# Optimization experiments

Measured on AMD Instinct MI355X. Metric: run time of the kernel, lower is better.

The kernel has to match this reference:

```python
import jax, jax.numpy as jnp
from jax import lax
import numpy as np

SEQ, BATCH, H, L = 4096, 64, 512, 2


def setup_inputs() -> dict:
    key = jax.random.key(0)
    ks = jax.random.split(key, 9)
    s = 1.0 / np.sqrt(H)  # PyTorch GRU init scale
    return {
        "x": jax.random.normal(ks[0], (SEQ, BATCH, 1), dtype=jnp.float32),
        "w_ih0": jax.random.normal(ks[1], (3 * H, 1), dtype=jnp.float32) * s,
        "w_hh0": jax.random.normal(ks[2], (3 * H, H), dtype=jnp.float32) * s,
        "b_ih0": jax.random.normal(ks[3], (3 * H,), dtype=jnp.float32) * s,
        "b_hh0": jax.random.normal(ks[4], (3 * H,), dtype=jnp.float32) * s,
        "w_ih1": jax.random.normal(ks[5], (3 * H, H), dtype=jnp.float32) * s,
        "w_hh1": jax.random.normal(ks[6], (3 * H, H), dtype=jnp.float32) * s,
        "b_ih1": jax.random.normal(ks[7], (3 * H,), dtype=jnp.float32) * s,
        "b_hh1": jax.random.normal(ks[8], (3 * H,), dtype=jnp.float32) * s,
    }


def _gru_layer(x_seq, w_ih, w_hh, b_ih, b_hh):
    """One GRU layer over time. x_seq: (T,B,I). Returns (outputs (T,B,H), h_T (B,H))."""
    h_dim = w_hh.shape[1]
    # Precompute input-side gate pre-activations for all timesteps (one big GEMM).
    gx = jnp.einsum('tbi,gi->tbg', x_seq, w_ih) + b_ih  # (T,B,3H)
    h0 = jnp.zeros((x_seq.shape[1], h_dim), dtype=x_seq.dtype)

    def step(h, gxt):
        gh = h @ w_hh.T + b_hh  # (B,3H)
        r = jax.nn.sigmoid(gxt[:, :h_dim] + gh[:, :h_dim])
        z = jax.nn.sigmoid(gxt[:, h_dim:2 * h_dim] + gh[:, h_dim:2 * h_dim])
        n = jnp.tanh(gxt[:, 2 * h_dim:] + r * gh[:, 2 * h_dim:])
        h_new = (1.0 - z) * n + z * h
        return h_new, h_new

    h_last, ys = lax.scan(step, h0, gx)
    return ys, h_last


def reference(x, w_ih0, w_hh0, b_ih0, b_hh0, w_ih1, w_hh1, b_ih1, b_hh1):
    y0, h0f = _gru_layer(x, w_ih0, w_hh0, b_ih0, b_hh0)
    _, h1f = _gru_layer(y0, w_ih1, w_hh1, b_ih1, b_hh1)
    # hidden: (num_layers, batch, hidden). Dropout is identity in eval mode.
    return jnp.stack([h0f, h1f], axis=0)
```

## Files before the change

### kernel.cpp

```cpp
#include <hip/hip_runtime.h>
#include <math.h>


#define TT 4096
#define BB 64
#define HH 512
#define NWG 256
#define PADU 32
#define HB32 (HH * BB)

typedef __attribute__((ext_vector_type(8))) short bf16x8;
typedef __attribute__((ext_vector_type(4))) float f32x4;
typedef unsigned long long ull;

#define MFMA16(a, b, c) __builtin_amdgcn_mfma_f32_16x16x32_bf16((a), (b), (c), 0, 0, 0)
#define RIDX(c) ((((c) >> 4) * 17) + ((c) & 15))

__device__ __forceinline__ float sigm(float v) { return 1.0f / (1.0f + expf(-v)); }

__device__ __forceinline__ unsigned aldu(const unsigned* p) {
    return __hip_atomic_load((unsigned*)p, __ATOMIC_RELAXED, __HIP_MEMORY_SCOPE_AGENT);
}
__device__ __forceinline__ void astu(unsigned* p, unsigned v) {
    __hip_atomic_store(p, v, __ATOMIC_RELAXED, __HIP_MEMORY_SCOPE_AGENT);
}
__device__ __forceinline__ ull ald64(const ull* p) {
    return __hip_atomic_load((ull*)p, __ATOMIC_RELAXED, __HIP_MEMORY_SCOPE_AGENT);
}
__device__ __forceinline__ unsigned short rneb(float f) {
    unsigned u = __float_as_uint(f);
    return (unsigned short)((u + 0x7fffu + ((u >> 16) & 1u)) >> 16);
}
__device__ __forceinline__ float bfhi_f(unsigned p) { return __uint_as_float(p & 0xffff0000u); }
__device__ __forceinline__ float bflo_f(unsigned p) { return __uint_as_float(p << 16); }

union frag_u { unsigned u[4]; bf16x8 v; };
__device__ __forceinline__ bf16x8 mkfrag(unsigned a, unsigned b, unsigned c, unsigned d) {
    frag_u x; x.u[0] = a; x.u[1] = b; x.u[2] = c; x.u[3] = d; return x.v;
}
__device__ __forceinline__ void wait_fence() {
    __builtin_amdgcn_sched_barrier(0);
    asm volatile("" ::: "memory");
}

__global__ __launch_bounds__(256) void zero_k(unsigned* p, int n) {
    int i = blockIdx.x * 256 + threadIdx.x;
    if (i < n) p[i] = 0u;
}

__global__ __launch_bounds__(256) void prep_aw0(const float* __restrict__ whh0,
                                                unsigned short* __restrict__ aw0) {
    int gid = blockIdx.x * 256 + threadIdx.x;
    if (gid >= 96 * 16 * 2 * 64) return;
    int lane = gid & 63, split = (gid >> 6) & 1, kt = (gid >> 7) & 15, rt = gid >> 11;
    int grow = (rt >> 5) * 512 + (rt & 31) * 16 + (lane & 15);
    int k0 = kt * 32 + (lane >> 4) * 8;
    #pragma unroll
    for (int i = 0; i < 8; ++i) {
        float val = whh0[(size_t)grow * 512 + k0 + i];
        unsigned short hb = rneb(val);
        unsigned short us = hb;
        if (split) us = rneb(val - __uint_as_float(((unsigned)hb) << 16));
        aw0[(size_t)gid * 8 + i] = us;
    }
}

__global__ __launch_bounds__(256) void prep_aw1(const float* __restrict__ wih1,
                                                const float* __restrict__ whh1,
                                                unsigned short* __restrict__ aw1) {
    int gid = blockIdx.x * 256 + threadIdx.x;
    if (gid >= 96 * 32 * 2 * 64) return;
    int lane = gid & 63, split = (gid >> 6) & 1, kt = (gid >> 7) & 31, rt = gid >> 12;
    int grow = (rt >> 5) * 512 + (rt & 31) * 16 + (lane & 15);
    #pragma unroll
    for (int i = 0; i < 8; ++i) {
        int k = kt * 32 + (lane >> 4) * 8 + i;
        float val = (k < 512) ? wih1[(size_t)grow * 512 + k]
                              : whh1[(size_t)grow * 512 + (k - 512)];
        unsigned short hb = rneb(val);
        unsigned short us = hb;
        if (split) us = rneb(val - __uint_as_float(((unsigned)hb) << 16));
        aw1[(size_t)gid * 8 + i] = us;
    }
}

#define ISSUE_KT(buf, src64, ktr)                                               \
    {                                                                           \
        _Pragma("unroll")                                                       \
        for (int i = 0; i < 4; ++i)                                             \
            buf[i] = ald64((src64) + ((ktr) * 16 + (l >> 4) * 4 + i) * 64       \
                           + bcol0);                                            \
    }

#define COMPUTE_KT(buf, kk)                                                     \
    {                                                                           \
        unsigned p0 = (unsigned)buf[0], p1 = (unsigned)(buf[0] >> 32);          \
        unsigned p2 = (unsigned)buf[1], p3 = (unsigned)(buf[1] >> 32);          \
        unsigned p4 = (unsigned)buf[2], p5 = (unsigned)(buf[2] >> 32);          \
        unsigned p6 = (unsigned)buf[3], p7 = (unsigned)(buf[3] >> 32);          \
        bf16x8 Bh = mkfrag(__builtin_amdgcn_perm(p1, p0, 0x07060302u),          \
                           __builtin_amdgcn_perm(p3, p2, 0x07060302u),          \
                           __builtin_amdgcn_perm(p5, p4, 0x07060302u),          \
                           __builtin_amdgcn_perm(p7, p6, 0x07060302u));         \
        bf16x8 Bl = mkfrag(__builtin_amdgcn_perm(p1, p0, 0x05040100u),          \
                           __builtin_amdgcn_perm(p3, p2, 0x05040100u),          \
                           __builtin_amdgcn_perm(p5, p4, 0x05040100u),          \
                           __builtin_amdgcn_perm(p7, p6, 0x05040100u));         \
        _Pragma("unroll")                                                       \
        for (int g = 0; g < 3; ++g) {                                           \
            acc[g] = MFMA16(wA[kk][g][0], Bh, acc[g]);                          \
            acc[g] = MFMA16(wA[kk][g][0], Bl, acc[g]);                          \
            acc[g] = MFMA16(wA[kk][g][1], Bh, acc[g]);                          \
        }                                                                       \
    }

__global__ __launch_bounds__(512, 1) void gru_persist(
    const float* __restrict__ x,
    const float* __restrict__ wih0,
    const float* __restrict__ bih0, const float* __restrict__ bhh0,
    const float* __restrict__ bih1, const float* __restrict__ bhh1,
    unsigned* __restrict__ ws)
{
    __shared__ float red[8][3][272];

    unsigned* r0 = ws;
    unsigned* r1 = ws + 4 * HB32;
    unsigned* flags = ws + 8 * HB32;
    const bf16x8* aw0f = (const bf16x8*)(ws + 8 * HB32 + NWG * PADU);
    const bf16x8* aw1f = aw0f + (size_t)96 * 16 * 2 * 64;

    const int tid = threadIdx.x;
    const int l   = tid & 63;
    const int w   = tid >> 6;
    const int id  = blockIdx.x;
    const int layer = id >> 7;
    const int jt  = (id >> 2) & 31;
    const int bq  = id & 3;
    const int bcol0 = bq * 16 + (l & 15);

    const int jl_e = tid >> 4;
    const int ce   = tid & 15;
    const int b_e  = bq * 16 + ce;
    const int rg_e = jl_e & 3;
    const int l_r  = ((jl_e >> 2) << 4) | ce;
    const int c_e  = RIDX(l_r * 4 + rg_e);
    const int jj   = jt * 16 + jl_e;
    const int hidx = ((jj >> 1) * 64 + b_e) * 2 + (jj & 1);

    unsigned fprod = 0, fguard = 0;

    if (layer == 0) {
        bf16x8 wA[2][3][2];
        #pragma unroll
        for (int kk = 0; kk < 2; ++kk)
            #pragma unroll
            for (int g = 0; g < 3; ++g)
                #pragma unroll
                for (int s = 0; s < 2; ++s)
                    wA[kk][g][s] = aw0f[(size_t)(((g * 32 + jt) * 16 + (2 * w + kk)) * 2 + s) * 64 + l];

        const float wir = wih0[jj], wiz = wih0[512 + jj], win = wih0[1024 + jj];
        const float br  = bih0[jj] + bhh0[jj];
        const float bz  = bih0[512 + jj] + bhh0[512 + jj];
        const float bnx = bih0[1024 + jj], bnh = bhh0[1024 + jj];

        for (int t = 0; t < TT; ++t) {
            const unsigned* hin  = r0 + ((t + 3) & 3) * HB32;
            unsigned*       hout = r0 + (t & 3) * HB32;
            const ull* hin64 = (const ull*)hin;

            unsigned po = aldu(hin + hidx);
            const float xv = x[(size_t)t * BB + b_e];

            if (l < 4) {
                const unsigned need = (unsigned)t;
                while (fprod < need) {
                    fprod = aldu(&flags[((4 * w + l) * 4 + bq) * PADU]);
                    if (fprod < need) __builtin_amdgcn_s_sleep(1);
                }
            }
            wait_fence();

            f32x4 acc[3];
            #pragma unroll
            for (int g = 0; g < 3; ++g) acc[g] = (f32x4){0.f, 0.f, 0.f, 0.f};

            ull bbA[4], bbB[4];
            ISSUE_KT(bbA, hin64, 2 * w)
            ISSUE_KT(bbB, hin64, 2 * w + 1)
            COMPUTE_KT(bbA, 0)
            COMPUTE_KT(bbB, 1)

            if (w == 4) {
                unsigned ng; int fidx;
                if (l < 32) { ng = (t >= 2) ? (unsigned)(t - 2) : 0u; fidx = l * 4 + bq; }
                else        { ng = (t >= 3) ? (unsigned)(t - 3) : 0u; fidx = 128 + (l - 32) * 4 + bq; }
                while (fguard < ng) {
                    fguard = aldu(&flags[fidx * PADU]);
                    if (fguard < ng) __builtin_amdgcn_s_sleep(1);
                }
            }
            wait_fence();

            #pragma unroll
            for (int g = 0; g < 3; ++g)
                *(f32x4*)&red[w][g][RIDX(l * 4)] = acc[g];
            __syncthreads();

            if (tid < 256) {
                float sr = 0.f, sz = 0.f, sn = 0.f;
                #pragma unroll
                for (int p = 0; p < 8; ++p) {
                    sr += red[p][0][c_e];
                    sz += red[p][1][c_e];
                    sn += red[p][2][c_e];
                }
                float r = sigm(xv * wir + br + sr);
                float z = sigm(xv * wiz + bz + sz);
                float n = tanhf(xv * win + bnx + r * (sn + bnh));
                float hn = (1.0f - z) * n + z * (bfhi_f(po) + bflo_f(po));
                unsigned hb = rneb(hn);
                unsigned lb = rneb(hn - __uint_as_float(hb << 16));
                astu(hout + hidx, (hb << 16) | lb);
            }
            __syncthreads();
            if (tid == 0) astu(&flags[id * PADU], (unsigned)(t + 1));
        }
    } else {
        bf16x8 wA[4][3][2];
        #pragma unroll
        for (int kk = 0; kk < 4; ++kk)
            #pragma unroll
            for (int g = 0; g < 3; ++g)
                #pragma unroll
                for (int s = 0; s < 2; ++s)
                    wA[kk][g][s] = aw1f[(size_t)(((g * 32 + jt) * 32 + (4 * w + kk)) * 2 + s) * 64 + l];

        const float br  = bih1[jj] + bhh1[jj];
        const float bz  = bih1[512 + jj] + bhh1[512 + jj];
        const float bnx = bih1[1024 + jj], bnh = bhh1[1024 + jj];
        const bool xside = (w < 4);

        for (int t = 1; t <= TT; ++t) {
            const unsigned* y0  = r0 + ((t + 3) & 3) * HB32;
            const unsigned* h1p = r1 + ((t + 2) & 3) * HB32;
            unsigned*       h1o = r1 + ((t + 3) & 3) * HB32;
            const ull* src64 = (const ull*)(xside ? y0 : h1p);
            const int kb = xside ? (4 * w) : (4 * (w - 4));

            unsigned po = aldu(h1p + hidx);

            if (l < 8) {
                unsigned need; int fidx;
                if (xside) { need = (unsigned)t;       fidx = (8 * w + l) * 4 + bq; }
                else       { need = (unsigned)(t - 1); fidx = 128 + (8 * (w - 4) + l) * 4 + bq; }
                while (fprod < need) {
                    fprod = aldu(&flags[fidx * PADU]);
                    if (fprod < need) __builtin_amdgcn_s_sleep(1);
                }
            }
            wait_fence();

            f32x4 acc[3];
            #pragma unroll
            for (int g = 0; g < 3; ++g) acc[g] = (f32x4){0.f, 0.f, 0.f, 0.f};

            ull bb0[4], bb1[4], bb2[4], bb3[4];
            ISSUE_KT(bb0, src64, kb + 0)
            ISSUE_KT(bb1, src64, kb + 1)
            ISSUE_KT(bb2, src64, kb + 2)
            ISSUE_KT(bb3, src64, kb + 3)
            COMPUTE_KT(bb0, 0)
            COMPUTE_KT(bb1, 1)
            COMPUTE_KT(bb2, 2)
            COMPUTE_KT(bb3, 3)

            if (w == 4 && l < 32) {
                const unsigned ng = (t >= 3) ? (unsigned)(t - 3) : 0u;
                while (fguard < ng) {
                    fguard = aldu(&flags[(128 + l * 4 + bq) * PADU]);
                    if (fguard < ng) __builtin_amdgcn_s_sleep(1);
                }
            }
            wait_fence();

            #pragma unroll
            for (int g = 0; g < 3; ++g)
                *(f32x4*)&red[w][g][RIDX(l * 4)] = acc[g];
            __syncthreads();

            if (tid < 256) {
                float sr = 0.f, sz = 0.f, sx = 0.f, sh = 0.f;
                #pragma unroll
                for (int p = 0; p < 4; ++p) {
                    sr += red[p][0][c_e];
                    sz += red[p][1][c_e];
                    sx += red[p][2][c_e];
                }
                #pragma unroll
                for (int p = 4; p < 8; ++p) {
                    sr += red[p][0][c_e];
                    sz += red[p][1][c_e];
                    sh += red[p][2][c_e];
                }
                float r = sigm(sr + br);
                float z = sigm(sz + bz);
                float n = tanhf(sx + bnx + r * (sh + bnh));
                float hn = (1.0f - z) * n + z * (bfhi_f(po) + bflo_f(po));
                unsigned hb = rneb(hn);
                unsigned lb = rneb(hn - __uint_as_float(hb << 16));
                astu(h1o + hidx, (hb << 16) | lb);
            }
            __syncthreads();
            if (tid == 0) astu(&flags[id * PADU], (unsigned)t);
        }
    }
}

__global__ __launch_bounds__(256) void copy_out_k(const unsigned* __restrict__ ws,
                                                  float* __restrict__ out) {
    int i = blockIdx.x * 256 + threadIdx.x;
    int lyr = i >> 15;
    int rem = i & 32767;
    int b = rem >> 9;
    int j = rem & 511;
    unsigned p = ws[(size_t)lyr * 4 * HB32 + 3 * HB32 + ((j >> 1) * 64 + b) * 2 + (j & 1)];
    out[i] = bfhi_f(p) + bflo_f(p);
}

extern "C" void kernel_launch(void* const* d_in, const int* in_sizes, int n_in,
                              void* d_out, int out_size, void* d_ws, size_t ws_size,
                              hipStream_t stream)
{
    const float* x    = (const float*)d_in[0];
    const float* wih0 = (const float*)d_in[1];
    const float* whh0 = (const float*)d_in[2];
    const float* bih0 = (const float*)d_in[3];
    const float* bhh0 = (const float*)d_in[4];
    const float* wih1 = (const float*)d_in[5];
    const float* whh1 = (const float*)d_in[6];
    const float* bih1 = (const float*)d_in[7];
    const float* bhh1 = (const float*)d_in[8];
    float* out = (float*)d_out;
    unsigned* ws = (unsigned*)d_ws;

    unsigned short* aw0 = (unsigned short*)(ws + 8 * HB32 + NWG * PADU);
    unsigned short* aw1 = aw0 + (size_t)96 * 16 * 2 * 64 * 8;

    const int nzero = 8 * HB32 + NWG * PADU;
    zero_k<<<(nzero + 255) / 256, 256, 0, stream>>>(ws, nzero);
    prep_aw0<<<(96 * 16 * 2 * 64) / 256, 256, 0, stream>>>(whh0, aw0);
    prep_aw1<<<(96 * 32 * 2 * 64) / 256, 256, 0, stream>>>(wih1, whh1, aw1);
    gru_persist<<<NWG, 512, 0, stream>>>(x, wih0, bih0, bhh0, bih1, bhh1, ws);
    copy_out_k<<<(2 * BB * HH) / 256, 256, 0, stream>>>(ws, out);
}
```

Baseline: 10.00 ms.

## Use per-wave completion flags and double-buffered LDS to drop trailing block barrier

Each of the four epilogue waves now publishes its own progress flag after draining its stores, instead of the whole block hitting a second __syncthreads and thread 0 writing one flag. Consumers poll four flags per producer block. The LDS reduction buffer is double-buffered by timestep parity so that removing the trailing barrier does not let the next step's partial sums overwrite data still being read. The goal is to shorten the per-step critical path in this persistent recurrent kernel, at the cost of four times more flag polling traffic and twice the LDS.

```diff
diff --git a/kernel.cpp b/kernel.cpp
--- a/kernel.cpp
+++ b/kernel.cpp
@@ -6,6 +6,7 @@
 #define BB 64
 #define HH 512
 #define NWG 256
+#define NFLAG (NWG * 4)
 #define PADU 32
 #define HB32 (HH * BB)
 
@@ -121,12 +122,12 @@
     const float* __restrict__ bih1, const float* __restrict__ bhh1,
     unsigned* __restrict__ ws)
 {
-    __shared__ float red[8][3][272];
+    __shared__ float red[2][8][3][272];
 
     unsigned* r0 = ws;
     unsigned* r1 = ws + 4 * HB32;
     unsigned* flags = ws + 8 * HB32;
-    const bf16x8* aw0f = (const bf16x8*)(ws + 8 * HB32 + NWG * PADU);
+    const bf16x8* aw0f = (const bf16x8*)(ws + 8 * HB32 + NFLAG * PADU);
     const bf16x8* aw1f = aw0f + (size_t)96 * 16 * 2 * 64;
 
     const int tid = threadIdx.x;
@@ -168,14 +169,16 @@
             const unsigned* hin  = r0 + ((t + 3) & 3) * HB32;
             unsigned*       hout = r0 + (t & 3) * HB32;
             const ull* hin64 = (const ull*)hin;
+            float (*redc)[3][272] = red[t & 1];
 
             unsigned po = aldu(hin + hidx);
             const float xv = x[(size_t)t * BB + b_e];
 
-            if (l < 4) {
+            if (l < 16) {
                 const unsigned need = (unsigned)t;
+                const int fidx = (((4 * w + (l >> 2)) * 4 + bq) * 4 + (l & 3)) * PADU;
                 while (fprod < need) {
-                    fprod = aldu(&flags[((4 * w + l) * 4 + bq) * PADU]);
+                    fprod = aldu(&flags[fidx]);
                     if (fprod < need) __builtin_amdgcn_s_sleep(1);
                 }
             }
@@ -193,8 +196,8 @@
 
             if (w == 4) {
                 unsigned ng; int fidx;
-                if (l < 32) { ng = (t >= 2) ? (unsigned)(t - 2) : 0u; fidx = l * 4 + bq; }
-                else        { ng = (t >= 3) ? (unsigned)(t - 3) : 0u; fidx = 128 + (l - 32) * 4 + bq; }
+                if (l < 32) { ng = (t >= 2) ? (unsigned)(t - 2) : 0u; fidx = (l * 4 + bq) * 4; }
+                else        { ng = (t >= 3) ? (unsigned)(t - 3) : 0u; fidx = ((128 + (l - 32) * 4 + bq)) * 4; }
                 while (fguard < ng) {
                     fguard = aldu(&flags[fidx * PADU]);
                     if (fguard < ng) __builtin_amdgcn_s_sleep(1);
@@ -204,16 +207,16 @@
 
             #pragma unroll
             for (int g = 0; g < 3; ++g)
-                *(f32x4*)&red[w][g][RIDX(l * 4)] = acc[g];
+                *(f32x4*)&redc[w][g][RIDX(l * 4)] = acc[g];
             __syncthreads();
 
             if (tid < 256) {
                 float sr = 0.f, sz = 0.f, sn = 0.f;
                 #pragma unroll
                 for (int p = 0; p < 8; ++p) {
-                    sr += red[p][0][c_e];
-                    sz += red[p][1][c_e];
-                    sn += red[p][2][c_e];
+                    sr += redc[p][0][c_e];
+                    sz += redc[p][1][c_e];
+                    sn += redc[p][2][c_e];
                 }
                 float r = sigm(xv * wir + br + sr);
                 float z = sigm(xv * wiz + bz + sz);
@@ -222,9 +225,9 @@
                 unsigned hb = rneb(hn);
                 unsigned lb = rneb(hn - __uint_as_float(hb << 16));
                 astu(hout + hidx, (hb << 16) | lb);
-            }
-            __syncthreads();
-            if (tid == 0) astu(&flags[id * PADU], (unsigned)(t + 1));
+                asm volatile("s_waitcnt vmcnt(0)" ::: "memory");
+                if (l == 0) astu(&flags[((id * 4) + w) * PADU], (unsigned)(t + 1));
+            }
         }
     } else {
         bf16x8 wA[4][3][2];
@@ -247,15 +250,17 @@
             unsigned*       h1o = r1 + ((t + 3) & 3) * HB32;
             const ull* src64 = (const ull*)(xside ? y0 : h1p);
             const int kb = xside ? (4 * w) : (4 * (w - 4));
+            float (*redc)[3][272] = red[t & 1];
 
             unsigned po = aldu(h1p + hidx);
 
-            if (l < 8) {
-                unsigned need; int fidx;
-                if (xside) { need = (unsigned)t;       fidx = (8 * w + l) * 4 + bq; }
-                else       { need = (unsigned)(t - 1); fidx = 128 + (8 * (w - 4) + l) * 4 + bq; }
+            if (l < 32) {
+                unsigned need; int pidx;
+                if (xside) { need = (unsigned)t;       pidx = (8 * w + (l >> 2)) * 4 + bq; }
+                else       { need = (unsigned)(t - 1); pidx = 128 + (8 * (w - 4) + (l >> 2)) * 4 + bq; }
+                const int fidx = (pidx * 4 + (l & 3)) * PADU;
                 while (fprod < need) {
-                    fprod = aldu(&flags[fidx * PADU]);
+                    fprod = aldu(&flags[fidx]);
                     if (fprod < need) __builtin_amdgcn_s_sleep(1);
                 }
             }
@@ -277,8 +282,9 @@
 
             if (w == 4 && l < 32) {
                 const unsigned ng = (t >= 3) ? (unsigned)(t - 3) : 0u;
+                const int fidx = ((128 + l * 4 + bq) * 4) * PADU;
                 while (fguard < ng) {
-                    fguard = aldu(&flags[(128 + l * 4 + bq) * PADU]);
+                    fguard = aldu(&flags[fidx]);
                     if (fguard < ng) __builtin_amdgcn_s_sleep(1);
                 }
             }
@@ -286,22 +292,22 @@
 
             #pragma unroll
             for (int g = 0; g < 3; ++g)
-                *(f32x4*)&red[w][g][RIDX(l * 4)] = acc[g];
+                *(f32x4*)&redc[w][g][RIDX(l * 4)] = acc[g];
             __syncthreads();
 
             if (tid < 256) {
                 float sr = 0.f, sz = 0.f, sx = 0.f, sh = 0.f;
                 #pragma unroll
                 for (int p = 0; p < 4; ++p) {
-                    sr += red[p][0][c_e];
-                    sz += red[p][1][c_e];
-                    sx += red[p][2][c_e];
+                    sr += redc[p][0][c_e];
+                    sz += redc[p][1][c_e];
+                    sx += redc[p][2][c_e];
                 }
                 #pragma unroll
                 for (int p = 4; p < 8; ++p) {
-                    sr += red[p][0][c_e];
-                    sz += red[p][1][c_e];
-                    sh += red[p][2][c_e];
+                    sr += redc[p][0][c_e];
+                    sz += redc[p][1][c_e];
+                    sh += redc[p][2][c_e];
                 }
                 float r = sigm(sr + br);
                 float z = sigm(sz + bz);
@@ -310,9 +316,9 @@
                 unsigned hb = rneb(hn);
                 unsigned lb = rneb(hn - __uint_as_float(hb << 16));
                 astu(h1o + hidx, (hb << 16) | lb);
-            }
-            __syncthreads();
-            if (tid == 0) astu(&flags[id * PADU], (unsigned)t);
+                asm volatile("s_waitcnt vmcnt(0)" ::: "memory");
+                if (l == 0) astu(&flags[((id * 4) + w) * PADU], (unsigned)t);
+            }
         }
     }
 }
@@ -344,10 +350,10 @@
     float* out = (float*)d_out;
     unsigned* ws = (unsigned*)d_ws;
 
-    unsigned short* aw0 = (unsigned short*)(ws + 8 * HB32 + NWG * PADU);
+    unsigned short* aw0 = (unsigned short*)(ws + 8 * HB32 + NFLAG * PADU);
     unsigned short* aw1 = aw0 + (size_t)96 * 16 * 2 * 64 * 8;
 
-    const int nzero = 8 * HB32 + NWG * PADU;
+    const int nzero = 8 * HB32 + NFLAG * PADU;
     zero_k<<<(nzero + 255) / 256, 256, 0, stream>>>(ws, nzero);
     prep_aw0<<<(96 * 16 * 2 * 64) / 256, 256, 0, stream>>>(whh0, aw0);
     prep_aw1<<<(96 * 32 * 2 * 64) / 256, 256, 0, stream>>>(wih1, whh1, aw1);
```

Result: slower. 18.30 ms (+83.0%).
